# Kernel tuning notes

Hardware: AMD Instinct MI355X
Metric: run time of the kernel (lower is better)

Reference implementation:

```python
import math
import jax, jax.numpy as jnp
import numpy as np

N = 10000      # num_nodes
E = 320000     # num_edges (avg degree 32)
D = 256        # hidden_dim
H = 8          # num_heads
HD = D // H    # head_dim = 32
S = 3          # num_scales
SCALES = (1.0, 2.0, 4.0)
BASE_MD = 500.0   # max_distance
RADIUS = 50.0     # spatial density radius


def setup_inputs() -> dict:
    key = jax.random.key(0)
    ks = jax.random.split(key, 24)
    nrm = lambda k, shape, s=0.02: jax.random.normal(k, shape, jnp.float32) * s
    return {
        "x": jax.random.normal(ks[0], (N, D), jnp.float32),
        "coords": jax.random.uniform(ks[1], (N, 2), jnp.float32) * 1000.0,
        "edge_index": jax.random.randint(ks[2], (2, E), 0, N, jnp.int32),
        "Wq": nrm(ks[3], (S, D, D)),
        "Wk": nrm(ks[4], (S, D, D)),
        "Wv": nrm(ks[5], (S, D, D)),
        "Wo": nrm(ks[6], (S, D, D)),
        "bo": jnp.zeros((S, D), jnp.float32),
        "temp": jnp.ones((S, H), jnp.float32),
        "dist_emb": nrm(ks[7], (S, 100, HD // 2)),
        "dir_emb": nrm(ks[8], (S, 16, HD // 2)),
        "Wsp1": nrm(ks[9], (S, HD, HD)),
        "bsp1": jnp.zeros((S, HD), jnp.float32),
        "Wsp2": nrm(ks[10], (S, 1, HD)),
        "bsp2": jnp.zeros((S, 1), jnp.float32),
        "Wd1": nrm(ks[11], (S, D // 2, 3)),
        "bd1": jnp.zeros((S, D // 2), jnp.float32),
        "Wd2": nrm(ks[12], (S, D, D // 2)),
        "bd2": jnp.zeros((S, D), jnp.float32),
        "Wf": nrm(ks[13], (D, S * D)),
        "bf": jnp.zeros((D,), jnp.float32),
    }


def reference(x, coords, edge_index, Wq, Wk, Wv, Wo, bo, temp, dist_emb, dir_emb,
              Wsp1, bsp1, Wsp2, bsp2, Wd1, bd1, Wd2, bd2, Wf, bf):
    src, dst = edge_index[0], edge_index[1]   # row=source j, col/dst=target i
    n = x.shape[0]
    eps = 1e-8

    # ---- shared density statistics (same math in every scale's encoder) ----
    ones_e = jnp.ones(src.shape[0], jnp.float32)
    deg = jax.ops.segment_sum(ones_e, src, num_segments=n)
    deg_n = deg / (deg.max() + eps)
    # spatial density: count of neighbors within RADIUS via full cdist (as in torch)
    c = jax.lax.stop_gradient(coords)  # only used via thresholds / integer bins -> zero grad
    d2 = jnp.sqrt(jnp.maximum(((c[:, None, :] - c[None, :, :]) ** 2).sum(-1), 0.0))
    sp = (d2 <= RADIUS).sum(axis=1).astype(jnp.float32) - 1.0
    sp = sp / (sp.max() + eps)
    # local feature variance
    nbr_sum = jax.ops.segment_sum(x[dst], src, num_segments=n)
    cnt = jnp.maximum(deg, 1.0)[:, None]
    fvar = jnp.linalg.norm(x - nbr_sum / cnt, axis=-1)
    fvar = fvar / (fvar.max() + eps)
    dens_raw = jnp.stack([deg_n, sp, fvar], axis=-1)  # [N, 3]

    # ---- shared relative geometry (binned -> no grad through coords) ----
    rel = c[src] - c[dst]                       # coords_j - coords_i
    dist = jnp.linalg.norm(rel, axis=-1)        # [E]
    ang = jnp.arctan2(rel[:, 1], rel[:, 0])
    abin = jnp.clip(((ang + math.pi) / (2.0 * math.pi) * 15.0).astype(jnp.int32), 0, 15)

    outs = []
    for s in range(S):
        md = BASE_MD * SCALES[s]
        dbin = jnp.clip((dist / md * 99.0).astype(jnp.int32), 0, 99)
        se = jnp.concatenate([dist_emb[s][dbin], dir_emb[s][abin]], axis=-1)  # [E, HD]
        enc = (jax.nn.relu(se @ Wsp1[s].T + bsp1[s]) @ Wsp2[s].T + bsp2[s])[:, 0]  # [E]

        df = jax.nn.relu(dens_raw @ Wd1[s].T + bd1[s]) @ Wd2[s].T + bd2[s]  # [N, D]

        q = (x @ Wq[s].T).reshape(n, H, HD)
        k = (x @ Wk[s].T).reshape(n, H, HD)
        v = (x @ Wv[s].T).reshape(n, H, HD)

        scores = (q[dst] * k[src]).sum(-1) / math.sqrt(HD)  # [E, H]
        scores = scores / temp[s][None, :]
        scores = scores + enc[:, None]
        dfi, dfj = df[dst], df[src]
        dsim = (dfi * dfj).sum(-1) / (jnp.maximum(jnp.linalg.norm(dfi, axis=-1), eps)
                                       * jnp.maximum(jnp.linalg.norm(dfj, axis=-1), eps))
        scores = scores * (1.0 + 0.5 * dsim[:, None])

        # scatter-softmax over edges grouped by destination node
        smax = jax.ops.segment_max(scores, dst, num_segments=n)
        p = jnp.exp(scores - smax[dst])
        z = jax.ops.segment_sum(p, dst, num_segments=n)
        probs = p / (z[dst] + 1e-16)

        agg = jax.ops.segment_sum(probs[..., None] * v[src], dst, num_segments=n)
        outs.append(agg.reshape(n, D) @ Wo[s].T + bo[s])

    fused = jnp.concatenate(outs, axis=-1) @ Wf.T + bf
    return fused
```

## Files before the change

### kernel.cpp

```cpp
#include <hip/hip_runtime.h>

typedef _Float16 f16;
typedef _Float16 f16x4 __attribute__((ext_vector_type(4)));
typedef _Float16 f16x8 __attribute__((ext_vector_type(8)));
typedef float    f32x4 __attribute__((ext_vector_type(4)));
typedef float    fv2   __attribute__((ext_vector_type(2)));

__device__ __forceinline__ float4 ld4h(const f16* p) {
  f16x4 t = *(const f16x4*)p;
  return make_float4((float)t[0], (float)t[1], (float)t[2], (float)t[3]);
}

__device__ __forceinline__ float4 dec_fp8x4(unsigned u) {
  fv2 lo = __builtin_amdgcn_cvt_pk_f32_fp8(u, false);
  fv2 hi = __builtin_amdgcn_cvt_pk_f32_fp8(u, true);
  return make_float4(lo[0], lo[1], hi[0], hi[1]);
}

__device__ __forceinline__ unsigned enc_fp8x4(float a, float b, float c, float d) {
  unsigned v = 0;
  v = __builtin_amdgcn_cvt_pk_fp8_f32(a, b, v, false);
  v = __builtin_amdgcn_cvt_pk_fp8_f32(c, d, v, true);
  return v;
}

__device__ __forceinline__ void gld_lds16(const void* g, void* l) {
  __builtin_amdgcn_global_load_lds(
      (const __attribute__((address_space(1))) unsigned*)g,
      (__attribute__((address_space(3))) unsigned*)l, 16, 0, 0);
}

__device__ __forceinline__ int cell_of(const float* coords, int i) {
  int cx = (int)(coords[2 * i] * 0.02f);
  int cy = (int)(coords[2 * i + 1] * 0.02f);
  cx = cx < 0 ? 0 : (cx > 19 ? 19 : cx);
  cy = cy < 0 ? 0 : (cy > 19 ? 19 : cy);
  return cy * 20 + cx;
}

__global__ __launch_bounds__(256) void prep_kernel(
    const float* __restrict__ x, const float* __restrict__ Wq, const float* __restrict__ Wk,
    const float* __restrict__ Wv, const float* __restrict__ Wd2,
    f16* __restrict__ x_h, unsigned* __restrict__ x8, f16* __restrict__ wqvk,
    f16* __restrict__ wd2h,
    const float* __restrict__ dist_emb, const float* __restrict__ dir_emb,
    const float* __restrict__ Wsp1, const float* __restrict__ bsp1,
    const float* __restrict__ Wsp2, const float* __restrict__ bsp2,
    float* __restrict__ enc_tab,
    const int* __restrict__ eidx, const float* __restrict__ coords,
    int* deg_i, int* indeg_i, int* cellcnt,
    const float* __restrict__ Wf, const float* __restrict__ Wo,
    const float* __restrict__ bo, const float* __restrict__ bf,
    f16* __restrict__ wfo, float* __restrict__ bias_f,
    int E, int N, int hb)
{
  const int b = blockIdx.x;
  if (b < 2048) {
    const int n0 = N * 64;
    const int total = n0 + 147456 + 24576;
    for (int i = b * 256 + threadIdx.x; i < total; i += 2048 * 256) {
      int k = i;
      if (k < n0) {
        float4 v = ((const float4*)x)[k];
        f16x4 o; o[0] = (f16)v.x; o[1] = (f16)v.y; o[2] = (f16)v.z; o[3] = (f16)v.w;
        ((f16x4*)x_h)[k] = o;
        x8[k] = enc_fp8x4(v.x, v.y, v.z, v.w);
        continue;
      }
      const float4* sp; f16x4* dp;
      k -= n0;
      if (k < 147456) {
        int s = k / 49152, r = k % 49152, m = r / 16384, off = r % 16384;
        const float* w = (m == 0) ? Wq : (m == 1) ? Wk : Wv;
        int dblk = (m == 0) ? 0 : (m == 1) ? 32768 : 16384;
        sp = (const float4*)(w + s * 65536) + off;
        dp = (f16x4*)wqvk + s * 49152 + dblk + off;
      } else {
        k -= 147456;
        sp = (const float4*)Wd2 + k; dp = (f16x4*)wd2h + k;
      }
      float4 v = *sp;
      f16x4 o; o[0] = (f16)v.x; o[1] = (f16)v.y; o[2] = (f16)v.z; o[3] = (f16)v.w;
      *dp = o;
    }
  } else if (b < 2067) {
    int id = (b - 2048) * 256 + threadIdx.x;
    if (id >= 3 * 1600) return;
    int s = id / 1600, c = id % 1600, db = c >> 4, ab = c & 15;
    const float* de = dist_emb + (size_t)(s * 100 + db) * 16;
    const float* ae = dir_emb + (size_t)(s * 16 + ab) * 16;
    const float* w1 = Wsp1 + s * 1024;
    const float* b1 = bsp1 + s * 32;
    const float* w2 = Wsp2 + s * 32;
    float enc = bsp2[s];
    for (int j = 0; j < 32; ++j) {
      float a = b1[j];
      const float* wr = w1 + j * 32;
#pragma unroll
      for (int i = 0; i < 16; ++i) a += de[i] * wr[i];
#pragma unroll
      for (int i = 0; i < 16; ++i) a += ae[i] * wr[16 + i];
      enc += fmaxf(a, 0.0f) * w2[j];
    }
    enc_tab[id] = enc;
  } else if (b < 2067 + hb) {
    int e = (b - 2067) * 256 + threadIdx.x;
    if (e < E) {
      atomicAdd(&deg_i[eidx[e]], 1);
      atomicAdd(&indeg_i[eidx[E + e]], 1);
    }
    if (e < N) atomicAdd(&cellcnt[cell_of(coords, e)], 1);
  } else if (b < 2067 + hb + 768) {
    __shared__ float wrow[256];
    int idx = b - (2067 + hb);
    int s = idx >> 8, o = idx & 255;
    int j = threadIdx.x;
    wrow[j] = Wf[o * 768 + s * 256 + j];
    __syncthreads();
    const float* wo = Wo + (size_t)s * 65536 + j;
    float acc = 0.f;
#pragma unroll 8
    for (int m = 0; m < 256; ++m) acc = fmaf(wrow[m], wo[(size_t)m * 256], acc);
    wfo[(size_t)o * 768 + s * 256 + j] = (f16)acc;
  } else {
    int j = threadIdx.x;
    float acc = bf[j];
    const float* wr = Wf + (size_t)j * 768;
    for (int t = 0; t < 768; ++t) acc = fmaf(bo[t], wr[t], acc);
    bias_f[j] = acc;
  }
}

__global__ __launch_bounds__(1024) void scan_kernel(const int* __restrict__ indeg,
                                                    const int* __restrict__ deg,
                                                    const int* __restrict__ cellcnt,
                                                    int* dptr, int* sptr, int* cptr,
                                                    int* __restrict__ perm, int N)
{
  __shared__ int lds[1024];
  __shared__ int cnt[256], scn2[256], fill[256];
  const int tid = threadIdx.x;
  const int pass = blockIdx.x;
  if (pass == 3) {
    if (tid < 256) { cnt[tid] = 0; fill[tid] = 0; }
    __syncthreads();
    for (int n = tid; n < N; n += 1024) {
      int d = indeg[n];
      int key = 255 - (d > 255 ? 255 : d);
      atomicAdd(&cnt[key], 1);
    }
    __syncthreads();
    if (tid < 256) scn2[tid] = cnt[tid];
    __syncthreads();
    for (int off = 1; off < 256; off <<= 1) {
      int v = 0;
      if (tid < 256 && tid >= off) v = scn2[tid - off];
      __syncthreads();
      if (tid < 256) scn2[tid] += v;
      __syncthreads();
    }
    for (int n = tid; n < N; n += 1024) {
      int d = indeg[n];
      int key = 255 - (d > 255 ? 255 : d);
      int pos = scn2[key] - cnt[key] + atomicAdd(&fill[key], 1);
      perm[pos] = n;
    }
    return;
  }
  const int* in = (pass == 0) ? indeg : (pass == 1) ? deg : cellcnt;
  int* out = (pass == 0) ? dptr : (pass == 1) ? sptr : cptr;
  int len = (pass == 2) ? 400 : N;
  int base = tid * 16;
  int loc[16];
  int sum = 0;
#pragma unroll
  for (int j = 0; j < 16; ++j) {
    int v = (base + j < len) ? in[base + j] : 0;
    loc[j] = sum; sum += v;
  }
  lds[tid] = sum;
  __syncthreads();
  for (int off = 1; off < 1024; off <<= 1) {
    int t = (tid >= off) ? lds[tid - off] : 0;
    __syncthreads();
    lds[tid] += t;
    __syncthreads();
  }
  int prev = tid ? lds[tid - 1] : 0;
#pragma unroll
  for (int j = 0; j < 16; ++j)
    if (base + j < len) out[base + j] = prev + loc[j];
  if (tid == 1023) out[len] = lds[1023];
}

__global__ __launch_bounds__(256) void scatter_kernel(
    const int* __restrict__ eidx, const float* __restrict__ coords,
    const int* __restrict__ dptr, const int* __restrict__ sptr, const int* __restrict__ cptr,
    int* fill_d, int* fill_s, int* fill_c,
    int2* __restrict__ erec, int* __restrict__ sdst, float2* __restrict__ scoord, int E, int N)
{
  int e = blockIdx.x * 256 + threadIdx.x;
  if (e < E) {
    int s = eidx[e], d = eidx[E + e];
    float rx = coords[2 * s] - coords[2 * d];
    float ry = coords[2 * s + 1] - coords[2 * d + 1];
    float dist = sqrtf(rx * rx + ry * ry);
    float ang = atan2f(ry, rx);
    int ab = (int)((ang + 3.14159265358979323846f) / 6.28318530717958647692f * 15.0f);
    ab = ab < 0 ? 0 : (ab > 15 ? 15 : ab);
    int b0 = (int)((dist / 500.0f) * 99.0f);  b0 = b0 < 0 ? 0 : (b0 > 99 ? 99 : b0);
    int b1 = (int)((dist / 1000.0f) * 99.0f); b1 = b1 < 0 ? 0 : (b1 > 99 ? 99 : b1);
    int b2 = (int)((dist / 2000.0f) * 99.0f); b2 = b2 < 0 ? 0 : (b2 > 99 ? 99 : b2);
    unsigned pb = (unsigned)b0 | ((unsigned)b1 << 7) | ((unsigned)b2 << 14) | ((unsigned)ab << 21);
    int pd = dptr[d] + atomicAdd(&fill_d[d], 1);
    erec[pd] = make_int2(s, (int)pb);
    int ps = sptr[s] + atomicAdd(&fill_s[s], 1);
    sdst[ps] = d;
  }
  if (e < N) {
    int cid = cell_of(coords, e);
    int pc = cptr[cid] + atomicAdd(&fill_c[cid], 1);
    scoord[pc] = ((const float2*)coords)[e];
  }
}

__global__ __launch_bounds__(256) void node_stats_kernel(
    const float* __restrict__ coords, const float2* __restrict__ scoord,
    const int* __restrict__ cptr,
    const float* __restrict__ x, const unsigned* __restrict__ x8,
    const int* __restrict__ sptr, const int* __restrict__ sdst,
    int* __restrict__ sp_i, float* __restrict__ fvar, int N)
{
  int wv = threadIdx.x >> 6, lane = threadIdx.x & 63;
  int node = blockIdx.x * 4 + wv;
  if (node >= N) return;

  float cx = coords[2 * node], cy = coords[2 * node + 1];
  {
    int gx = (int)(cx * 0.02f); gx = gx < 0 ? 0 : (gx > 19 ? 19 : gx);
    int gy = (int)(cy * 0.02f); gy = gy < 0 ? 0 : (gy > 19 ? 19 : gy);
    int x0 = gx > 0 ? gx - 1 : 0, x1 = gx < 19 ? gx + 1 : 19;
    int y0 = gy > 0 ? gy - 1 : 0, y1 = gy < 19 ? gy + 1 : 19;
    int cnt = 0;
    for (int r = y0; r <= y1; ++r) {
      int j0 = cptr[r * 20 + x0], j1 = cptr[r * 20 + x1 + 1];
      for (int j = j0 + lane; j < j1; j += 64) {
        float2 c = scoord[j];
        float dx = cx - c.x, dy = cy - c.y;
        cnt += (dx * dx + dy * dy <= 2500.0f) ? 1 : 0;
      }
    }
    cnt += __shfl_xor(cnt, 1);  cnt += __shfl_xor(cnt, 2);  cnt += __shfl_xor(cnt, 4);
    cnt += __shfl_xor(cnt, 8);  cnt += __shfl_xor(cnt, 16); cnt += __shfl_xor(cnt, 32);
    if (lane == 0) sp_i[node] = cnt;
  }

  const int slot = lane >> 3, w = lane & 7;
  float sum[32];
#pragma unroll
  for (int i = 0; i < 32; ++i) sum[i] = 0.f;
  int e0 = sptr[node], e1 = sptr[node + 1];
  int nit = (e1 - e0 + 7) >> 3;
  for (int it = 0; it < nit; ++it) {
    int e = e0 + it * 8 + slot;
    bool valid = e < e1;
    int dd = sdst[valid ? e : e1 - 1];
    const unsigned* xp = x8 + dd * 64 + w * 8;
    uint4 a = *(const uint4*)xp;
    uint4 b = *(const uint4*)(xp + 4);
    float vm = valid ? 1.f : 0.f;
    unsigned wd[8] = {a.x, a.y, a.z, a.w, b.x, b.y, b.z, b.w};
#pragma unroll
    for (int k = 0; k < 8; ++k) {
      float4 f = dec_fp8x4(wd[k]);
      sum[k*4+0] = fmaf(vm, f.x, sum[k*4+0]);
      sum[k*4+1] = fmaf(vm, f.y, sum[k*4+1]);
      sum[k*4+2] = fmaf(vm, f.z, sum[k*4+2]);
      sum[k*4+3] = fmaf(vm, f.w, sum[k*4+3]);
    }
  }
#pragma unroll
  for (int i = 0; i < 32; ++i) {
    sum[i] += __shfl_xor(sum[i], 8);
    sum[i] += __shfl_xor(sum[i], 16);
    sum[i] += __shfl_xor(sum[i], 32);
  }
  float rcnt = 1.0f / fmaxf((float)(e1 - e0), 1.0f);
  const float4* xp4 = (const float4*)(x + (size_t)node * 256 + w * 32);
  float ss = 0.f;
#pragma unroll
  for (int k = 0; k < 8; ++k) {
    float4 xm = xp4[k];
    float d0 = xm.x - sum[k*4+0] * rcnt;
    float d1 = xm.y - sum[k*4+1] * rcnt;
    float d2 = xm.z - sum[k*4+2] * rcnt;
    float d3 = xm.w - sum[k*4+3] * rcnt;
    ss += d0*d0 + d1*d1 + d2*d2 + d3*d3;
  }
  ss += __shfl_xor(ss, 1);  ss += __shfl_xor(ss, 2);  ss += __shfl_xor(ss, 4);
  ss += __shfl_xor(ss, 8);  ss += __shfl_xor(ss, 16); ss += __shfl_xor(ss, 32);
  if (lane == 0) fvar[node] = sqrtf(ss * 0.125f);
}

__global__ __launch_bounds__(1024) void maxred_kernel(
    const int* __restrict__ sptr, const int* __restrict__ sp_i,
    const float* __restrict__ fvar, float* __restrict__ maxf, int N)
{
  __shared__ float l0[1024], l1[1024], l2[1024];
  int tid = threadIdx.x;
  float m0 = 0.f, m1 = 0.f, m2 = 0.f;
  for (int i = tid; i < N; i += 1024) {
    m0 = fmaxf(m0, (float)(sptr[i + 1] - sptr[i]));
    m1 = fmaxf(m1, (float)(sp_i[i] - 1));
    m2 = fmaxf(m2, fvar[i]);
  }
  l0[tid] = m0; l1[tid] = m1; l2[tid] = m2;
  __syncthreads();
  for (int off = 512; off > 0; off >>= 1) {
    if (tid < off) {
      l0[tid] = fmaxf(l0[tid], l0[tid + off]);
      l1[tid] = fmaxf(l1[tid], l1[tid + off]);
      l2[tid] = fmaxf(l2[tid], l2[tid + off]);
    }
    __syncthreads();
  }
  if (tid == 0) { maxf[0] = l0[0]; maxf[1] = l1[0]; maxf[2] = l2[0]; }
}

__global__ __launch_bounds__(256) void gemm_wd2(
    const int* __restrict__ sptr, const int* __restrict__ sp_i, const float* __restrict__ fvar,
    const float* __restrict__ maxf, const float* __restrict__ Wd1, const float* __restrict__ bd1,
    const f16* __restrict__ B, const float* __restrict__ bd2,
    f16* __restrict__ dfh, int N, int Mp)
{
  __shared__ f16 As[128 * 64];
  __shared__ f16 Bs[128 * 64];
  const int s = blockIdx.z;
  const int tid = threadIdx.x;
  const int lane = tid & 63;
  const int w = tid >> 6;
  const int wr = (w >> 1) * 64, wc = (w & 1) * 64;
  const int srow = tid >> 3;
  const int c = tid & 7;
  const int scolB = ((c ^ (srow & 7))) * 8;
  const f16* Bb = B + (size_t)s * 32768 + (size_t)(blockIdx.y * 128 + srow) * 128 + scolB;
  char* Bsl = (char*)Bs + tid * 16;
  const float dm = maxf[0] + 1e-8f, sm = maxf[1] + 1e-8f, fm = maxf[2] + 1e-8f;

  f32x4 acc[4][4] = {};

  for (int kt = 0; kt < 128; kt += 64) {
    __syncthreads();
#pragma unroll
    for (int i = 0; i < 4; ++i)
      gld_lds16(Bb + (size_t)i * 32 * 128 + kt, Bsl + i * 4096);
#pragma unroll
    for (int i = 0; i < 4; ++i) {
      int r = srow + i * 32;
      int node = blockIdx.x * 128 + r;
      float d0 = 0.f, d1 = 0.f, d2 = 0.f;
      if (node < N) {
        d0 = (float)(sptr[node + 1] - sptr[node]) / dm;
        d1 = (float)(sp_i[node] - 1) / sm;
        d2 = fvar[node] / fm;
      }
      int kc8 = c ^ (r & 7);
      const float* w1 = Wd1 + s * 384 + (kt + kc8 * 8) * 3;
      const float* b1 = bd1 + s * 128 + kt + kc8 * 8;
      f16x8 hv;
#pragma unroll
      for (int j = 0; j < 8; ++j) {
        float h = fmaf(w1[j*3], d0, fmaf(w1[j*3+1], d1, fmaf(w1[j*3+2], d2, b1[j])));
        hv[j] = (f16)fmaxf(h, 0.f);
      }
      *(f16x8*)&As[r * 64 + c * 8] = hv;
    }
    __syncthreads();
#pragma unroll
    for (int kq = 0; kq < 2; ++kq) {
      const int krd = kq * 32 + (lane >> 4) * 8;
      const int kc = krd >> 3;
      f16x8 af[4], bfr[4];
#pragma unroll
      for (int t = 0; t < 4; ++t) {
        const int ra = wr + t * 16 + (lane & 15);
        const int rb = wc + t * 16 + (lane & 15);
        af[t]  = *(const f16x8*)&As[ra * 64 + (kc ^ (ra & 7)) * 8];
        bfr[t] = *(const f16x8*)&Bs[rb * 64 + (kc ^ (rb & 7)) * 8];
      }
#pragma unroll
      for (int mi = 0; mi < 4; ++mi)
#pragma unroll
        for (int ni = 0; ni < 4; ++ni)
          acc[mi][ni] = __builtin_amdgcn_mfma_f32_16x16x32_f16(af[mi], bfr[ni], acc[mi][ni], 0, 0, 0);
    }
  }

  const int r0 = (lane >> 4) << 2;
  const int c0 = lane & 15;
#pragma unroll
  for (int mi = 0; mi < 4; ++mi) {
#pragma unroll
    for (int ni = 0; ni < 4; ++ni) {
      int col = blockIdx.y * 128 + wc + ni * 16 + c0;
      float bv = bd2[s * 256 + col];
#pragma unroll
      for (int r = 0; r < 4; ++r) {
        int row = blockIdx.x * 128 + wr + mi * 16 + r0 + r;
        dfh[(size_t)s * Mp * 256 + (size_t)row * 256 + col] = (f16)(acc[mi][ni][r] + bv);
      }
    }
  }
}

__global__ __launch_bounds__(256) void gemm_bt_f16(
    const f16* __restrict__ A, int lda, long sA,
    const f16* __restrict__ B, int ldb, long sB,
    const float* __restrict__ bias, int sBias,
    void* __restrict__ Cv, int ldc, long sC, int K, int Mstore, int outMode,
    unsigned char* __restrict__ Cv2, int ldc2, long sC2, int ysplit)
{
  __shared__ f16 As[128 * 64];
  __shared__ f16 Bs[128 * 64];
  const int s = blockIdx.z;
  const int tid = threadIdx.x;
  const int lane = tid & 63;
  const int w = tid >> 6;
  const int wr = (w >> 1) * 64, wc = (w & 1) * 64;
  const int srow = tid >> 3;
  const int scol = (((tid & 7) ^ (srow & 7))) * 8;
  const f16* Ab = A + (size_t)s * sA + (size_t)(blockIdx.x * 128 + srow) * lda + scol;
  const f16* Bb = B + (size_t)s * sB + (size_t)(blockIdx.y * 128 + srow) * ldb + scol;
  char* Asl = (char*)As + tid * 16;
  char* Bsl = (char*)Bs + tid * 16;

  f32x4 acc[4][4] = {};

  for (int kt = 0; kt < K; kt += 64) {
    __syncthreads();
#pragma unroll
    for (int i = 0; i < 4; ++i) {
      gld_lds16(Ab + (size_t)i * 32 * lda + kt, Asl + i * 4096);
      gld_lds16(Bb + (size_t)i * 32 * ldb + kt, Bsl + i * 4096);
    }
    __syncthreads();
#pragma unroll
    for (int kq = 0; kq < 2; ++kq) {
      const int krd = kq * 32 + (lane >> 4) * 8;
      const int kc = krd >> 3;
      f16x8 af[4], bfr[4];
#pragma unroll
      for (int t = 0; t < 4; ++t) {
        const int ra = wr + t * 16 + (lane & 15);
        const int rb = wc + t * 16 + (lane & 15);
        af[t]  = *(const f16x8*)&As[ra * 64 + (kc ^ (ra & 7)) * 8];
        bfr[t] = *(const f16x8*)&Bs[rb * 64 + (kc ^ (rb & 7)) * 8];
      }
#pragma unroll
      for (int mi = 0; mi < 4; ++mi)
#pragma unroll
        for (int ni = 0; ni < 4; ++ni)
          acc[mi][ni] = __builtin_amdgcn_mfma_f32_16x16x32_f16(af[mi], bfr[ni], acc[mi][ni], 0, 0, 0);
    }
  }

  const int r0 = (lane >> 4) << 2;
  const int c0 = lane & 15;
  const bool f8p = ((int)blockIdx.y >= ysplit);
  const int cbase = f8p ? ((int)blockIdx.y - ysplit) * 128 : (int)blockIdx.y * 128;
#pragma unroll
  for (int mi = 0; mi < 4; ++mi) {
#pragma unroll
    for (int ni = 0; ni < 4; ++ni) {
      int col = cbase + wc + ni * 16 + c0;
      float bv = (!f8p && bias) ? bias[s * sBias + col] : 0.0f;
#pragma unroll
      for (int r = 0; r < 4; ++r) {
        int row = blockIdx.x * 128 + wr + mi * 16 + r0 + r;
        if (row < Mstore) {
          float v = acc[mi][ni][r] + bv;
          if (f8p) {
            unsigned pk = __builtin_amdgcn_cvt_pk_fp8_f32(v, v, 0u, false);
            Cv2[(size_t)s * sC2 + (size_t)row * ldc2 + col] = (unsigned char)(pk & 0xffu);
          } else if (outMode == 1) {
            ((f16*)Cv)[(size_t)s * sC + (size_t)row * ldc + col] = (f16)v;
          } else {
            ((float*)Cv)[(size_t)s * sC + (size_t)row * ldc + col] = v;
          }
        }
      }
    }
  }
}

__global__ __launch_bounds__(256) void norm_kernel(const f16* __restrict__ dfh,
                                                   unsigned* __restrict__ drec8, int N, int Mp)
{
  int wv = threadIdx.x >> 6, lane = threadIdx.x & 63;
  int node = blockIdx.x * 4 + wv;
  if (node >= N) return;
  int s = blockIdx.y;
  float4 d = ld4h(dfh + (size_t)s * Mp * 256 + (size_t)node * 256 + lane * 4);
  float ss = d.x * d.x + d.y * d.y + d.z * d.z + d.w * d.w;
  ss += __shfl_xor(ss, 1);  ss += __shfl_xor(ss, 2);  ss += __shfl_xor(ss, 4);
  ss += __shfl_xor(ss, 8);  ss += __shfl_xor(ss, 16); ss += __shfl_xor(ss, 32);
  float rn = 1.0f / fmaxf(sqrtf(ss), 1e-8f);
  drec8[(size_t)s * Mp * 64 + node * 64 + lane] = enc_fp8x4(d.x * rn, d.y * rn, d.z * rn, d.w * rn);
}

__global__ __launch_bounds__(256) void edge_attn(
    const f16* __restrict__ nrec0, const unsigned* __restrict__ krec0,
    const unsigned* __restrict__ drec0, const int2* __restrict__ erec,
    const int* __restrict__ dptr, const int* __restrict__ perm,
    const float* __restrict__ enc_tab, const float* __restrict__ temp,
    f16* __restrict__ aggc, int N, int Mp)
{
  int wv = threadIdx.x >> 6, lane = threadIdx.x & 63;
  int node = blockIdx.x * 4 + wv;
  if (node >= N) return;
  node = perm[node];
  const int s = blockIdx.y;
  const int sshift = 7 * s;
  const f16* nrec = nrec0 + (size_t)s * Mp * 512;
  const unsigned* krec8 = krec0 + (size_t)s * Mp * 64;
  const unsigned* drec8 = drec0 + (size_t)s * Mp * 64;
  const float* enc_s = enc_tab + s * 1600;

  const int slot = lane >> 4;
  const int sub  = lane & 15;
  const int hd   = sub >> 1;
  const int half = sub & 1;
  const int doff = hd * 8 + half * 4;
  const int voff = hd * 32 + half * 16;

  float qf[16];
  {
    const f16* qp = nrec + (size_t)node * 512 + voff;
    f16x8 a = *(const f16x8*)qp;
    f16x8 b = *(const f16x8*)(qp + 8);
#pragma unroll
    for (int j = 0; j < 8; ++j) { qf[j] = (float)a[j]; qf[8 + j] = (float)b[j]; }
  }
  uint4 diw = *(const uint4*)(drec8 + node * 64 + doff);
  const float inv_th = 0.17677669529663687f / temp[s * 8 + hd];

  float m = -1e30f, z = 0.f;
  float acc[16];
#pragma unroll
  for (int i = 0; i < 16; ++i) acc[i] = 0.f;

  int e0 = dptr[node], e1 = dptr[node + 1];
  int nit = (e1 - e0 + 3) >> 2;
  if (nit > 0) {
    int ce = e0 + slot; if (ce >= e1) ce = e1 - 1;
    int2 recA = erec[ce];
    for (int it = 0; it < nit; ++it) {
      int en = e0 + (it + 1) * 4 + slot; en = (en < e1) ? en : e1 - 1;
      int2 recN = erec[en];

      int e = e0 + it * 4 + slot;
      bool valid = e < e1;
      int src = recA.x;
      unsigned pb = (unsigned)recA.y;
      uint4 kwv = *(const uint4*)(krec8 + src * 64 + doff);
      uint4 dwv = *(const uint4*)(drec8 + src * 64 + doff);
      const f16* vp = nrec + (size_t)src * 512 + 256 + voff;
      f16x8 vs0 = *(const f16x8*)vp;
      f16x8 vs1 = *(const f16x8*)(vp + 8);
      float enc = enc_s[((pb >> sshift) & 127u) * 16 + (pb >> 21)];

      unsigned kw[4] = {kwv.x, kwv.y, kwv.z, kwv.w};
      unsigned dw[4] = {dwv.x, dwv.y, dwv.z, dwv.w};
      unsigned di[4] = {diw.x, diw.y, diw.z, diw.w};
      float qk0 = 0.f, qk1 = 0.f, ds0 = 0.f, ds1 = 0.f;
#pragma unroll
      for (int w = 0; w < 4; ++w) {
        float4 kf = dec_fp8x4(kw[w]);
        qk0 = fmaf(qf[w*4+0], kf.x, qk0);
        qk1 = fmaf(qf[w*4+1], kf.y, qk1);
        qk0 = fmaf(qf[w*4+2], kf.z, qk0);
        qk1 = fmaf(qf[w*4+3], kf.w, qk1);
        float4 df = dec_fp8x4(dw[w]);
        float4 dd = dec_fp8x4(di[w]);
        ds0 = fmaf(dd.x, df.x, ds0);
        ds1 = fmaf(dd.y, df.y, ds1);
        ds0 = fmaf(dd.z, df.z, ds0);
        ds1 = fmaf(dd.w, df.w, ds1);
      }
      float qk = qk0 + qk1;
      float ds = ds0 + ds1;
      qk += __shfl_xor(qk, 1);
      ds += __shfl_xor(ds, 1); ds += __shfl_xor(ds, 2);
      ds += __shfl_xor(ds, 4); ds += __shfl_xor(ds, 8);

      float sc = (qk * inv_th + enc) * (1.0f + 0.5f * ds);
      sc = valid ? sc : -1e30f;
      if (__any(sc > m + 8.0f)) {
        float mn = fmaxf(m, sc);
        float rs = __expf(m - mn);
        z *= rs;
#pragma unroll
        for (int i = 0; i < 16; ++i) acc[i] *= rs;
        m = mn;
      }
      float p = __expf(sc - m) * (valid ? 1.0f : 0.0f);
      z += p;
#pragma unroll
      for (int j = 0; j < 8; ++j) acc[j]     = fmaf(p, (float)vs0[j], acc[j]);
#pragma unroll
      for (int j = 0; j < 8; ++j) acc[8 + j] = fmaf(p, (float)vs1[j], acc[8 + j]);

      recA = recN;
    }
  }

  float M = m;
  M = fmaxf(M, __shfl_xor(M, 16));
  M = fmaxf(M, __shfl_xor(M, 32));
  float f = __expf(m - M);
  z *= f;
  z += __shfl_xor(z, 16); z += __shfl_xor(z, 32);
#pragma unroll
  for (int i = 0; i < 16; ++i) {
    float a = acc[i] * f;
    a += __shfl_xor(a, 16); a += __shfl_xor(a, 32);
    acc[i] = a;
  }
  float rz = 1.0f / (z + 1e-16f);
  if (slot == 0) {
    f16* op = aggc + (size_t)node * 768 + s * 256 + voff;
    f16x8 o0, o1;
#pragma unroll
    for (int j = 0; j < 8; ++j) { o0[j] = (f16)(acc[j] * rz); o1[j] = (f16)(acc[8 + j] * rz); }
    *(f16x8*)op = o0;
    *(f16x8*)(op + 8) = o1;
  }
}

extern "C" void kernel_launch(void* const* d_in, const int* in_sizes, int n_in,
                              void* d_out, int out_size, void* d_ws, size_t ws_size,
                              hipStream_t stream)
{
  const float* x      = (const float*)d_in[0];
  const float* coords = (const float*)d_in[1];
  const int*   eidx   = (const int*)  d_in[2];
  const float* Wq   = (const float*)d_in[3];
  const float* Wk   = (const float*)d_in[4];
  const float* Wv   = (const float*)d_in[5];
  const float* Wo   = (const float*)d_in[6];
  const float* bo   = (const float*)d_in[7];
  const float* temp = (const float*)d_in[8];
  const float* dist_emb = (const float*)d_in[9];
  const float* dir_emb  = (const float*)d_in[10];
  const float* Wsp1 = (const float*)d_in[11];
  const float* bsp1 = (const float*)d_in[12];
  const float* Wsp2 = (const float*)d_in[13];
  const float* bsp2 = (const float*)d_in[14];
  const float* Wd1  = (const float*)d_in[15];
  const float* bd1  = (const float*)d_in[16];
  const float* Wd2  = (const float*)d_in[17];
  const float* bd2  = (const float*)d_in[18];
  const float* Wf   = (const float*)d_in[19];
  const float* bf   = (const float*)d_in[20];
  (void)n_in; (void)out_size; (void)ws_size;

  const int N  = in_sizes[0] / 256;
  const int E  = in_sizes[2] / 2;
  const int Mp = ((N + 127) / 128) * 128;

  char* p = (char*)d_ws;
  auto alloc = [&](size_t b) -> void* {
    void* r = (void*)p;
    p += (b + 255) & ~(size_t)255;
    return r;
  };

  f16*      x_h   = (f16*)     alloc((size_t)Mp * 256 * 2);
  unsigned* x8    = (unsigned*)alloc((size_t)Mp * 256);
  f16*      nrec3 = (f16*)     alloc((size_t)3 * Mp * 512 * 2);
  unsigned* krec3 = (unsigned*)alloc((size_t)3 * Mp * 256);
  unsigned* drec3 = (unsigned*)alloc((size_t)3 * Mp * 256);
  f16*      dfh3  = (f16*)     alloc((size_t)3 * Mp * 256 * 2);
  f16*      aggc  = (f16*)     alloc((size_t)Mp * 768 * 2);
  f16*      wqvk  = (f16*)     alloc((size_t)3 * 768 * 256 * 2);
  f16*      wfo   = (f16*)     alloc((size_t)256 * 768 * 2);
  float*    bias_f = (float*)  alloc(256 * 4);
  f16*      wd2h  = (f16*)     alloc((size_t)3 * 256 * 128 * 2);
  float*    enc_tab = (float*) alloc((size_t)3 * 1600 * 4);
  int*    dptr = (int*)   alloc((size_t)(N + 1) * 4);
  int*    sptr = (int*)   alloc((size_t)(N + 1) * 4);
  int*    cptr = (int*)   alloc((size_t)401 * 4);
  int*    perm = (int*)   alloc((size_t)N * 4);
  int2*   erec = (int2*)  alloc((size_t)E * 8);
  int*    sdst = (int*)   alloc((size_t)E * 4);
  float2* scoord = (float2*)alloc((size_t)N * 8);
  float*  fvar = (float*) alloc((size_t)N * 4);
  int*    sp_i = (int*)   alloc((size_t)N * 4);
  float*  maxf = (float*) alloc(4 * 4);
  char* z0 = p;
  int* deg_i   = (int*)alloc((size_t)N * 4);
  int* indeg_i = (int*)alloc((size_t)N * 4);
  int* fill_d  = (int*)alloc((size_t)N * 4);
  int* fill_s  = (int*)alloc((size_t)N * 4);
  int* cellcnt = (int*)alloc(400 * 4);
  int* fill_c  = (int*)alloc(400 * 4);
  size_t zbytes = (size_t)(p - z0);
  hipMemsetAsync(z0, 0, zbytes, stream);

  const int hb = (E + 255) / 256;
  prep_kernel<<<2067 + hb + 768 + 1, 256, 0, stream>>>(
      x, Wq, Wk, Wv, Wd2, x_h, x8, wqvk, wd2h,
      dist_emb, dir_emb, Wsp1, bsp1, Wsp2, bsp2, enc_tab,
      eidx, coords, deg_i, indeg_i, cellcnt,
      Wf, Wo, bo, bf, wfo, bias_f, E, N, hb);
  scan_kernel<<<4, 1024, 0, stream>>>(indeg_i, deg_i, cellcnt, dptr, sptr, cptr, perm, N);
  scatter_kernel<<<(E + 255) / 256, 256, 0, stream>>>(eidx, coords, dptr, sptr, cptr,
                                                      fill_d, fill_s, fill_c, erec, sdst, scoord, E, N);
  node_stats_kernel<<<(N + 3) / 4, 256, 0, stream>>>(coords, scoord, cptr, x, x8,
                                                     sptr, sdst, sp_i, fvar, N);
  maxred_kernel<<<1, 1024, 0, stream>>>(sptr, sp_i, fvar, maxf, N);

  const int mtiles = Mp / 128;
  gemm_wd2<<<dim3(mtiles, 2, 3), 256, 0, stream>>>(sptr, sp_i, fvar, maxf, Wd1, bd1,
                                                   wd2h, bd2, dfh3, N, Mp);
  norm_kernel<<<dim3((N + 3) / 4, 3), 256, 0, stream>>>(dfh3, drec3, N, Mp);
  gemm_bt_f16<<<dim3(mtiles, 6, 3), 256, 0, stream>>>(x_h, 256, 0,
                                                      wqvk, 256, 196608, nullptr, 0,
                                                      nrec3, 512, (long)Mp * 512, 256, Mp, 1,
                                                      (unsigned char*)krec3, 256, (long)Mp * 256, 4);
  edge_attn<<<dim3((N + 3) / 4, 3), 256, 0, stream>>>(nrec3, krec3, drec3, erec, dptr, perm,
                                                      enc_tab, temp, aggc, N, Mp);
  gemm_bt_f16<<<dim3(mtiles, 2, 1), 256, 0, stream>>>(aggc, 768, 0,
                                                      wfo, 768, 0, bias_f, 0,
                                                      d_out, 256, 0, 768, N, 0,
                                                      nullptr, 0, 0, 99);
}
```

Before: 336.3 us.

## Co-schedule QKV GEMM with node stats in one launch; batch Wf·Wo fold

The QKV projection GEMM blocks and the node statistics work are merged into one launch, with blocks picking their role from the block index. The two independent workloads can then overlap on the GPU, and one launch plus its serialization point goes away. The Wf·Wo weight-folding pass in prep_kernel now computes 8 output rows per block instead of 1, reusing each Wo load 8 times and cutting those blocks from 768 to 96. The merged kernel's node-stat blocks now reserve the GEMM's 32 KB of LDS, which may lower their occupancy.

```diff
diff --git a/kernel.cpp b/kernel.cpp
--- a/kernel.cpp
+++ b/kernel.cpp
@@ -36,6 +36,84 @@
   cx = cx < 0 ? 0 : (cx > 19 ? 19 : cx);
   cy = cy < 0 ? 0 : (cy > 19 ? 19 : cy);
   return cy * 20 + cx;
+}
+
+__device__ __forceinline__ void gemm_core(
+    f16* As, f16* Bs, int bx, int by, int s,
+    const f16* __restrict__ A, int lda, long sA,
+    const f16* __restrict__ B, int ldb, long sB,
+    const float* __restrict__ bias, int sBias,
+    void* __restrict__ Cv, int ldc, long sC, int K, int Mstore, int outMode,
+    unsigned char* __restrict__ Cv2, int ldc2, long sC2, int ysplit)
+{
+  const int tid = threadIdx.x;
+  const int lane = tid & 63;
+  const int w = tid >> 6;
+  const int wr = (w >> 1) * 64, wc = (w & 1) * 64;
+  const int srow = tid >> 3;
+  const int scol = (((tid & 7) ^ (srow & 7))) * 8;
+  const f16* Ab = A + (size_t)s * sA + (size_t)(bx * 128 + srow) * lda + scol;
+  const f16* Bb = B + (size_t)s * sB + (size_t)(by * 128 + srow) * ldb + scol;
+  char* Asl = (char*)As + tid * 16;
+  char* Bsl = (char*)Bs + tid * 16;
+
+  f32x4 acc[4][4] = {};
+
+  for (int kt = 0; kt < K; kt += 64) {
+    __syncthreads();
+#pragma unroll
+    for (int i = 0; i < 4; ++i) {
+      gld_lds16(Ab + (size_t)i * 32 * lda + kt, Asl + i * 4096);
+      gld_lds16(Bb + (size_t)i * 32 * ldb + kt, Bsl + i * 4096);
+    }
+    __syncthreads();
+#pragma unroll
+    for (int kq = 0; kq < 2; ++kq) {
+      const int krd = kq * 32 + (lane >> 4) * 8;
+      const int kc = krd >> 3;
+      f16x8 af[4], bfr[4];
+#pragma unroll
+      for (int t = 0; t < 4; ++t) {
+        const int ra = wr + t * 16 + (lane & 15);
+        const int rb = wc + t * 16 + (lane & 15);
+        af[t]  = *(const f16x8*)&As[ra * 64 + (kc ^ (ra & 7)) * 8];
+        bfr[t] = *(const f16x8*)&Bs[rb * 64 + (kc ^ (rb & 7)) * 8];
+      }
+#pragma unroll
+      for (int mi = 0; mi < 4; ++mi)
+#pragma unroll
+        for (int ni = 0; ni < 4; ++ni)
+          acc[mi][ni] = __builtin_amdgcn_mfma_f32_16x16x32_f16(af[mi], bfr[ni], acc[mi][ni], 0, 0, 0);
+    }
+  }
+
+  const int r0 = (lane >> 4) << 2;
+  const int c0 = lane & 15;
+  const bool f8p = (by >= ysplit);
+  const int cbase = f8p ? (by - ysplit) * 128 : by * 128;
+#pragma unroll
+  for (int mi = 0; mi < 4; ++mi) {
+#pragma unroll
+    for (int ni = 0; ni < 4; ++ni) {
+      int col = cbase + wc + ni * 16 + c0;
+      float bv = (!f8p && bias) ? bias[s * sBias + col] : 0.0f;
+#pragma unroll
+      for (int r = 0; r < 4; ++r) {
+        int row = bx * 128 + wr + mi * 16 + r0 + r;
+        if (row < Mstore) {
+          float v = acc[mi][ni][r] + bv;
+          if (f8p) {
+            unsigned pk = __builtin_amdgcn_cvt_pk_fp8_f32(v, v, 0u, false);
+            Cv2[(size_t)s * sC2 + (size_t)row * ldc2 + col] = (unsigned char)(pk & 0xffu);
+          } else if (outMode == 1) {
+            ((f16*)Cv)[(size_t)s * sC + (size_t)row * ldc + col] = (f16)v;
+          } else {
+            ((float*)Cv)[(size_t)s * sC + (size_t)row * ldc + col] = v;
+          }
+        }
+      }
+    }
+  }
 }
 
 __global__ __launch_bounds__(256) void prep_kernel(
@@ -110,18 +188,25 @@
       atomicAdd(&indeg_i[eidx[E + e]], 1);
     }
     if (e < N) atomicAdd(&cellcnt[cell_of(coords, e)], 1);
-  } else if (b < 2067 + hb + 768) {
-    __shared__ float wrow[256];
+  } else if (b < 2067 + hb + 96) {
+    __shared__ float wf8[8][256];
     int idx = b - (2067 + hb);
-    int s = idx >> 8, o = idx & 255;
+    int s = idx / 32;
+    int og = (idx % 32) * 8;
     int j = threadIdx.x;
-    wrow[j] = Wf[o * 768 + s * 256 + j];
+#pragma unroll
+    for (int oo = 0; oo < 8; ++oo) wf8[oo][j] = Wf[(og + oo) * 768 + s * 256 + j];
     __syncthreads();
     const float* wo = Wo + (size_t)s * 65536 + j;
-    float acc = 0.f;
-#pragma unroll 8
-    for (int m = 0; m < 256; ++m) acc = fmaf(wrow[m], wo[(size_t)m * 256], acc);
-    wfo[(size_t)o * 768 + s * 256 + j] = (f16)acc;
+    float acc[8] = {0.f, 0.f, 0.f, 0.f, 0.f, 0.f, 0.f, 0.f};
+    for (int m = 0; m < 256; ++m) {
+      float val = wo[(size_t)m * 256];
+#pragma unroll
+      for (int oo = 0; oo < 8; ++oo) acc[oo] = fmaf(wf8[oo][m], val, acc[oo]);
+    }
+#pragma unroll
+    for (int oo = 0; oo < 8; ++oo)
+      wfo[(size_t)(og + oo) * 768 + s * 256 + j] = (f16)acc[oo];
   } else {
     int j = threadIdx.x;
     float acc = bf[j];
@@ -224,15 +309,30 @@
   }
 }
 
-__global__ __launch_bounds__(256) void node_stats_kernel(
+__global__ __launch_bounds__(256) void mid_kernel(
+    const f16* __restrict__ x_h, const f16* __restrict__ wqvk,
+    f16* __restrict__ nrec3, unsigned char* __restrict__ krec3,
     const float* __restrict__ coords, const float2* __restrict__ scoord,
     const int* __restrict__ cptr,
     const float* __restrict__ x, const unsigned* __restrict__ x8,
     const int* __restrict__ sptr, const int* __restrict__ sdst,
-    int* __restrict__ sp_i, float* __restrict__ fvar, int N)
-{
+    int* __restrict__ sp_i, float* __restrict__ fvar,
+    int N, int Mp, int mtiles, int qkvB)
+{
+  __shared__ f16 As[128 * 64];
+  __shared__ f16 Bs[128 * 64];
+  const int b = blockIdx.x;
+  if (b < qkvB) {
+    int bx = b % mtiles;
+    int t = b / mtiles;
+    gemm_core(As, Bs, bx, t % 6, t / 6,
+              x_h, 256, 0, wqvk, 256, 196608, nullptr, 0,
+              nrec3, 512, (long)Mp * 512, 256, Mp, 1,
+              krec3, 256, (long)Mp * 256, 4);
+    return;
+  }
   int wv = threadIdx.x >> 6, lane = threadIdx.x & 63;
-  int node = blockIdx.x * 4 + wv;
+  int node = (b - qkvB) * 4 + wv;
   if (node >= N) return;
 
   float cx = coords[2 * node], cy = coords[2 * node + 1];
@@ -267,9 +367,9 @@
     int dd = sdst[valid ? e : e1 - 1];
     const unsigned* xp = x8 + dd * 64 + w * 8;
     uint4 a = *(const uint4*)xp;
-    uint4 b = *(const uint4*)(xp + 4);
+    uint4 bq = *(const uint4*)(xp + 4);
     float vm = valid ? 1.f : 0.f;
-    unsigned wd[8] = {a.x, a.y, a.z, a.w, b.x, b.y, b.z, b.w};
+    unsigned wd[8] = {a.x, a.y, a.z, a.w, bq.x, bq.y, bq.z, bq.w};
 #pragma unroll
     for (int k = 0; k < 8; ++k) {
       float4 f = dec_fp8x4(wd[k]);
@@ -422,75 +522,9 @@
 {
   __shared__ f16 As[128 * 64];
   __shared__ f16 Bs[128 * 64];
-  const int s = blockIdx.z;
-  const int tid = threadIdx.x;
-  const int lane = tid & 63;
-  const int w = tid >> 6;
-  const int wr = (w >> 1) * 64, wc = (w & 1) * 64;
-  const int srow = tid >> 3;
-  const int scol = (((tid & 7) ^ (srow & 7))) * 8;
-  const f16* Ab = A + (size_t)s * sA + (size_t)(blockIdx.x * 128 + srow) * lda + scol;
-  const f16* Bb = B + (size_t)s * sB + (size_t)(blockIdx.y * 128 + srow) * ldb + scol;
-  char* Asl = (char*)As + tid * 16;
-  char* Bsl = (char*)Bs + tid * 16;
-
-  f32x4 acc[4][4] = {};
-
-  for (int kt = 0; kt < K; kt += 64) {
-    __syncthreads();
-#pragma unroll
-    for (int i = 0; i < 4; ++i) {
-      gld_lds16(Ab + (size_t)i * 32 * lda + kt, Asl + i * 4096);
-      gld_lds16(Bb + (size_t)i * 32 * ldb + kt, Bsl + i * 4096);
-    }
-    __syncthreads();
-#pragma unroll
-    for (int kq = 0; kq < 2; ++kq) {
-      const int krd = kq * 32 + (lane >> 4) * 8;
-      const int kc = krd >> 3;
-      f16x8 af[4], bfr[4];
-#pragma unroll
-      for (int t = 0; t < 4; ++t) {
-        const int ra = wr + t * 16 + (lane & 15);
-        const int rb = wc + t * 16 + (lane & 15);
-        af[t]  = *(const f16x8*)&As[ra * 64 + (kc ^ (ra & 7)) * 8];
-        bfr[t] = *(const f16x8*)&Bs[rb * 64 + (kc ^ (rb & 7)) * 8];
-      }
-#pragma unroll
-      for (int mi = 0; mi < 4; ++mi)
-#pragma unroll
-        for (int ni = 0; ni < 4; ++ni)
-          acc[mi][ni] = __builtin_amdgcn_mfma_f32_16x16x32_f16(af[mi], bfr[ni], acc[mi][ni], 0, 0, 0);
-    }
-  }
-
-  const int r0 = (lane >> 4) << 2;
-  const int c0 = lane & 15;
-  const bool f8p = ((int)blockIdx.y >= ysplit);
-  const int cbase = f8p ? ((int)blockIdx.y - ysplit) * 128 : (int)blockIdx.y * 128;
-#pragma unroll
-  for (int mi = 0; mi < 4; ++mi) {
-#pragma unroll
-    for (int ni = 0; ni < 4; ++ni) {
-      int col = cbase + wc + ni * 16 + c0;
-      float bv = (!f8p && bias) ? bias[s * sBias + col] : 0.0f;
-#pragma unroll
-      for (int r = 0; r < 4; ++r) {
-        int row = blockIdx.x * 128 + wr + mi * 16 + r0 + r;
-        if (row < Mstore) {
-          float v = acc[mi][ni][r] + bv;
-          if (f8p) {
-            unsigned pk = __builtin_amdgcn_cvt_pk_fp8_f32(v, v, 0u, false);
-            Cv2[(size_t)s * sC2 + (size_t)row * ldc2 + col] = (unsigned char)(pk & 0xffu);
-          } else if (outMode == 1) {
-            ((f16*)Cv)[(size_t)s * sC + (size_t)row * ldc + col] = (f16)v;
-          } else {
-            ((float*)Cv)[(size_t)s * sC + (size_t)row * ldc + col] = v;
-          }
-        }
-      }
-    }
-  }
+  gemm_core(As, Bs, blockIdx.x, blockIdx.y, blockIdx.z,
+            A, lda, sA, B, ldb, sB, bias, sBias,
+            Cv, ldc, sC, K, Mstore, outMode, Cv2, ldc2, sC2, ysplit);
 }
 
 __global__ __launch_bounds__(256) void norm_kernel(const f16* __restrict__ dfh,
@@ -708,7 +742,7 @@
   hipMemsetAsync(z0, 0, zbytes, stream);
 
   const int hb = (E + 255) / 256;
-  prep_kernel<<<2067 + hb + 768 + 1, 256, 0, stream>>>(
+  prep_kernel<<<2067 + hb + 96 + 1, 256, 0, stream>>>(
       x, Wq, Wk, Wv, Wd2, x_h, x8, wqvk, wd2h,
       dist_emb, dir_emb, Wsp1, bsp1, Wsp2, bsp2, enc_tab,
       eidx, coords, deg_i, indeg_i, cellcnt,
@@ -716,18 +750,16 @@
   scan_kernel<<<4, 1024, 0, stream>>>(indeg_i, deg_i, cellcnt, dptr, sptr, cptr, perm, N);
   scatter_kernel<<<(E + 255) / 256, 256, 0, stream>>>(eidx, coords, dptr, sptr, cptr,
                                                       fill_d, fill_s, fill_c, erec, sdst, scoord, E, N);
-  node_stats_kernel<<<(N + 3) / 4, 256, 0, stream>>>(coords, scoord, cptr, x, x8,
-                                                     sptr, sdst, sp_i, fvar, N);
+  const int mtiles = Mp / 128;
+  const int qkvB = mtiles * 18;
+  mid_kernel<<<qkvB + (N + 3) / 4, 256, 0, stream>>>(
+      x_h, wqvk, nrec3, (unsigned char*)krec3,
+      coords, scoord, cptr, x, x8, sptr, sdst, sp_i, fvar,
+      N, Mp, mtiles, qkvB);
   maxred_kernel<<<1, 1024, 0, stream>>>(sptr, sp_i, fvar, maxf, N);
-
-  const int mtiles = Mp / 128;
   gemm_wd2<<<dim3(mtiles, 2, 3), 256, 0, stream>>>(sptr, sp_i, fvar, maxf, Wd1, bd1,
                                                    wd2h, bd2, dfh3, N, Mp);
   norm_kernel<<<dim3((N + 3) / 4, 3), 256, 0, stream>>>(dfh3, drec3, N, Mp);
-  gemm_bt_f16<<<dim3(mtiles, 6, 3), 256, 0, stream>>>(x_h, 256, 0,
-                                                      wqvk, 256, 196608, nullptr, 0,
-                                                      nrec3, 512, (long)Mp * 512, 256, Mp, 1,
-                                                      (unsigned char*)krec3, 256, (long)Mp * 256, 4);
   edge_attn<<<dim3((N + 3) / 4, 3), 256, 0, stream>>>(nrec3, krec3, drec3, erec, dptr, perm,
                                                       enc_tab, temp, aggc, N, Mp);
   gemm_bt_f16<<<dim3(mtiles, 2, 1), 256, 0, stream>>>(aggc, 768, 0,
```

New measurement: 332.2 us. Within noise of the previous version (-1.2%).
